# Kernel tuning notes

Measured on AMD Instinct MI355X. Metric: run time of the kernel, lower is better.

The kernel has to match this reference:

```python
import jax, jax.numpy as jnp
import numpy as np

B, T, D, H = 4, 2048, 1024, 16
Dh = D // H


def setup_inputs() -> dict:
    key = jax.random.key(0)
    ks = jax.random.split(key, 10)
    s = 0.02  # init scale for weights
    return {
        "x": jax.random.normal(ks[0], (B, T, D), jnp.float32),
        "gates": jax.random.uniform(ks[1], (B, H), jnp.float32),
        "Wq": jax.random.normal(ks[2], (D, D), jnp.float32) * s,
        "bq": jnp.zeros((D,), jnp.float32),
        "Wk": jax.random.normal(ks[3], (D, D), jnp.float32) * s,
        "bk": jnp.zeros((D,), jnp.float32),
        "Wv": jax.random.normal(ks[4], (D, D), jnp.float32) * s,
        "bv": jnp.zeros((D,), jnp.float32),
        "Wo": jax.random.normal(ks[5], (D, D), jnp.float32) * s,
        "bo": jnp.zeros((D,), jnp.float32),
    }


def reference(x, gates, Wq, bq, Wk, bk, Wv, bv, Wo, bo):
    # x: [B,T,D], gates: [B,H]. torch Linear is y = x @ W.T + b.
    b, t, d = x.shape
    h = gates.shape[1]
    dh = d // h
    q = (x @ Wq.T + bq).reshape(b, t, h, dh)
    k = (x @ Wk.T + bk).reshape(b, t, h, dh)
    v = (x @ Wv.T + bv).reshape(b, t, h, dh)
    scores = jnp.einsum('bthd,bshd->bhts', q, k) / jnp.sqrt(jnp.float32(dh))
    A = jax.nn.softmax(scores, axis=-1)
    A = A * gates[:, :, None, None]  # post-softmax per-head gate
    z = jnp.einsum('bhts,bshd->bthd', A, v).reshape(b, t, d)
    out = z @ Wo.T + bo
    return out, A
```

## Files before the change

### kernel.cpp

```cpp
#include <hip/hip_runtime.h>

#define BB 4
#define TT 2048
#define DD 1024
#define HH 16
#define DHH 64

using half8  = __attribute__((ext_vector_type(8))) _Float16;
using half4v = __attribute__((ext_vector_type(4))) _Float16;
using f32x4  = __attribute__((ext_vector_type(4))) float;

#define EXP2C 0.18033688011112042f

__device__ __forceinline__ float fexp2(float x) {
#if __has_builtin(__builtin_amdgcn_exp2f)
  return __builtin_amdgcn_exp2f(x);
#else
  return exp2f(x);
#endif
}

__device__ __forceinline__ void gload_lds16(const _Float16* g, _Float16* l) {
  __builtin_amdgcn_global_load_lds((const __attribute__((address_space(1))) void*)g,
                                   (__attribute__((address_space(3))) void*)l, 16, 0, 0);
}

__global__ void cvt_all(const float* __restrict__ x,
                        const float* __restrict__ wq, const float* __restrict__ wk,
                        const float* __restrict__ wv, const float* __restrict__ wo,
                        _Float16* __restrict__ xh,
                        _Float16* __restrict__ wqh, _Float16* __restrict__ wkh,
                        _Float16* __restrict__ wvh, _Float16* __restrict__ woh) {
  const float* s; _Float16* d; int n8, b0, nb;
  int b = blockIdx.x;
  if (b < 512) { s = x; d = xh; n8 = BB * TT * DD / 8; b0 = b; nb = 512; }
  else {
    int wsel = (b - 512) >> 6;
    b0 = (b - 512) & 63; nb = 64; n8 = DD * DD / 8;
    s = wsel == 0 ? wq : wsel == 1 ? wk : wsel == 2 ? wv : wo;
    d = wsel == 0 ? wqh : wsel == 1 ? wkh : wsel == 2 ? wvh : woh;
  }
  for (int i = b0 * 256 + threadIdx.x; i < n8; i += nb * 256) {
    const float4* p = (const float4*)(s + (size_t)i * 8);
    float4 a = p[0], bb = p[1];
    half8 h;
    h[0] = (_Float16)a.x; h[1] = (_Float16)a.y; h[2] = (_Float16)a.z; h[3] = (_Float16)a.w;
    h[4] = (_Float16)bb.x; h[5] = (_Float16)bb.y; h[6] = (_Float16)bb.z; h[7] = (_Float16)bb.w;
    *(half8*)(d + (size_t)i * 8) = h;
  }
}

template <int MODE>
__global__ __launch_bounds__(256, 2) void gemm_nt(const _Float16* __restrict__ A,
                                                  const _Float16* __restrict__ Bw,
                                                  const float* __restrict__ bias,
                                                  void* __restrict__ Cout) {
  constexpr int K = 1024;
  __shared__ _Float16 As[2][128 * 64];
  __shared__ _Float16 Bs[2][128 * 64];
  const int tid = threadIdx.x;
  const int l = tid & 63, w = tid >> 6;
  const int wm = w >> 1, wn = w & 1;
  const int lg = l >> 4, lr16 = l & 15;
  const int row0 = blockIdx.x * 128, col0 = blockIdx.y * 128;

  f32x4 acc[4][4];
#pragma unroll
  for (int i = 0; i < 4; ++i)
#pragma unroll
    for (int j = 0; j < 4; ++j) acc[i][j] = (f32x4)0.0f;

#define GEMM_STAGE(K0, BSEL)                                                        \
  _Pragma("unroll") for (int it = 0; it < 4; ++it) {                                \
    int chunk = tid + it * 256;                                                     \
    int r = chunk >> 3, pb = chunk & 7, lb = pb ^ (r & 7);                          \
    gload_lds16(A + (size_t)(row0 + r) * K + (K0) * 64 + lb * 8, As[BSEL] + chunk * 8);  \
    gload_lds16(Bw + (size_t)(col0 + r) * K + (K0) * 64 + lb * 8, Bs[BSEL] + chunk * 8); \
  }

  GEMM_STAGE(0, 0);
  int cur = 0;
  for (int k0 = 0; k0 < 16; ++k0) {
    __syncthreads();
    if (k0 < 15) GEMM_STAGE(k0 + 1, cur ^ 1);
#pragma unroll
    for (int kb = 0; kb < 2; ++kb) {
      half8 a[4], b[4];
#pragma unroll
      for (int f = 0; f < 4; ++f) {
        int ar = wm * 64 + f * 16 + lr16;
        a[f] = *(const half8*)(As[cur] + ar * 64 + ((kb * 4 + lg) ^ (ar & 7)) * 8);
        int br = wn * 64 + f * 16 + lr16;
        b[f] = *(const half8*)(Bs[cur] + br * 64 + ((kb * 4 + lg) ^ (br & 7)) * 8);
      }
#pragma unroll
      for (int i = 0; i < 4; ++i)
#pragma unroll
        for (int j = 0; j < 4; ++j)
          acc[i][j] = __builtin_amdgcn_mfma_f32_16x16x32_f16(a[i], b[j], acc[i][j], 0, 0, 0);
    }
    cur ^= 1;
  }

#pragma unroll
  for (int fi = 0; fi < 4; ++fi) {
#pragma unroll
    for (int fj = 0; fj < 4; ++fj) {
      int gi0 = row0 + wm * 64 + fi * 16 + lg * 4;
      int gj = col0 + wn * 64 + fj * 16 + lr16;
      float bj = bias[gj];
      if constexpr (MODE == 2) {
        float* O = (float*)Cout;
#pragma unroll
        for (int r = 0; r < 4; ++r) O[(size_t)(gi0 + r) * DD + gj] = acc[fi][fj][r] + bj;
      } else if constexpr (MODE == 1) {
        _Float16* O = (_Float16*)Cout;
        int b = gi0 >> 11, t0 = gi0 & 2047;
        int h = gj >> 6, dh = gj & 63;
        half4v tmp;
#pragma unroll
        for (int r = 0; r < 4; ++r) tmp[r] = (_Float16)(acc[fi][fj][r] + bj);
        *(half4v*)(O + (((size_t)(b * HH + h) * DHH + dh) * TT + t0)) = tmp;
      } else {
        _Float16* O = (_Float16*)Cout;
        int b = gi0 >> 11, t0 = gi0 & 2047;
        int h = gj >> 6, dh = gj & 63;
#pragma unroll
        for (int r = 0; r < 4; ++r)
          O[(((size_t)(b * HH + h) * TT + (t0 + r)) << 6) + dh] = (_Float16)(acc[fi][fj][r] + bj);
      }
    }
  }
}

__global__ __launch_bounds__(512, 2) void attn_kernel(const _Float16* __restrict__ qh,
                                                      const _Float16* __restrict__ kh,
                                                      const _Float16* __restrict__ vTh,
                                                      const float* __restrict__ gates,
                                                      float* __restrict__ Aout,
                                                      _Float16* __restrict__ zh) {
  __shared__ _Float16 Qs[128 * 64];
  __shared__ _Float16 Ks[2][64 * 64];
  __shared__ _Float16 Vs[2][64 * 64];
  __shared__ _Float16 Ps[128 * 64];
  const int tid = threadIdx.x;
  const int l = tid & 63, w = tid >> 6;
  const int lg = l >> 4, lr16 = l & 15;
  const int wr0 = w * 16;
  const int blk = ((int)blockIdx.x & 7) * 128 + ((int)blockIdx.x >> 3);
  const int rt = blk & 15, bh = blk >> 4;
  const _Float16* Qp = qh + (size_t)bh * TT * DHH + (size_t)rt * 128 * DHH;
  const _Float16* Kp = kh + (size_t)bh * TT * DHH;
  const _Float16* Vp = vTh + (size_t)bh * DHH * TT;
  float* Ap = Aout + (size_t)bh * TT * TT + (size_t)rt * 128 * TT;
  const float gate = gates[bh];

#pragma unroll
  for (int it = 0; it < 2; ++it) {
    int chunk = tid + it * 512;
    int r = chunk >> 3, pb = chunk & 7, lb = pb ^ (r & 7);
    gload_lds16(Qp + (size_t)r * DHH + lb * 8, Qs + chunk * 8);
  }

#define STAGE_K(CT, BSEL) {                                                   \
    int chunk = tid; int r = chunk >> 3, pb = chunk & 7, lb = pb ^ (r & 7);   \
    gload_lds16(Kp + (size_t)((CT) * 64 + r) * DHH + lb * 8, Ks[BSEL] + chunk * 8); }
#define STAGE_V(CT, BSEL) {                                                   \
    int chunk = tid; int r = chunk >> 3, pb = chunk & 7, lb = pb ^ (r & 7);   \
    gload_lds16(Vp + (size_t)r * TT + (CT) * 64 + lb * 8, Vs[BSEL] + chunk * 8); }

  STAGE_K(0, 0);
  float rs[4] = {0.f, 0.f, 0.f, 0.f};
  int cur = 0;
  for (int ct = 0; ct < 32; ++ct) {
    __syncthreads();
    if (ct < 31) STAGE_K(ct + 1, cur ^ 1);
    f32x4 s[4];
#pragma unroll
    for (int j = 0; j < 4; ++j) s[j] = (f32x4)0.0f;
#pragma unroll
    for (int kb = 0; kb < 2; ++kb) {
      int qr = wr0 + lr16;
      half8 aQ = *(const half8*)(Qs + qr * 64 + (((kb * 4 + lg) ^ (qr & 7)) * 8));
      half8 bK[4];
#pragma unroll
      for (int fc = 0; fc < 4; ++fc) {
        int kr = fc * 16 + lr16;
        bK[fc] = *(const half8*)(Ks[cur] + kr * 64 + (((kb * 4 + lg) ^ (kr & 7)) * 8));
      }
#pragma unroll
      for (int fc = 0; fc < 4; ++fc)
        s[fc] = __builtin_amdgcn_mfma_f32_16x16x32_f16(aQ, bK[fc], s[fc], 0, 0, 0);
    }
#pragma unroll
    for (int fc = 0; fc < 4; ++fc)
#pragma unroll
      for (int r = 0; r < 4; ++r) rs[r] += fexp2(s[fc][r] * EXP2C);
    cur ^= 1;
  }

  float inv[4];
#pragma unroll
  for (int r = 0; r < 4; ++r) {
    float v = rs[r];
    v += __shfl_xor(v, 1, 64);
    v += __shfl_xor(v, 2, 64);
    v += __shfl_xor(v, 4, 64);
    v += __shfl_xor(v, 8, 64);
    inv[r] = gate / v;
  }

  f32x4 z[4];
#pragma unroll
  for (int j = 0; j < 4; ++j) z[j] = (f32x4)0.0f;
  STAGE_K(0, 0);
  STAGE_V(0, 0);
  cur = 0;
  for (int ct = 0; ct < 32; ++ct) {
    __syncthreads();
    if (ct < 31) {
      STAGE_K(ct + 1, cur ^ 1);
      STAGE_V(ct + 1, cur ^ 1);
    }
    f32x4 s[4];
#pragma unroll
    for (int j = 0; j < 4; ++j) s[j] = (f32x4)0.0f;
#pragma unroll
    for (int kb = 0; kb < 2; ++kb) {
      int qr = wr0 + lr16;
      half8 aQ = *(const half8*)(Qs + qr * 64 + (((kb * 4 + lg) ^ (qr & 7)) * 8));
      half8 bK[4];
#pragma unroll
      for (int fc = 0; fc < 4; ++fc) {
        int kr = fc * 16 + lr16;
        bK[fc] = *(const half8*)(Ks[cur] + kr * 64 + (((kb * 4 + lg) ^ (kr & 7)) * 8));
      }
#pragma unroll
      for (int fc = 0; fc < 4; ++fc)
        s[fc] = __builtin_amdgcn_mfma_f32_16x16x32_f16(aQ, bK[fc], s[fc], 0, 0, 0);
    }
    const int rbase = wr0 + lg * 4;
#pragma unroll
    for (int fc = 0; fc < 4; ++fc) {
      int lc = fc * 16 + lr16;
#pragma unroll
      for (int r = 0; r < 4; ++r) {
        float av = fexp2(s[fc][r] * EXP2C) * inv[r];
        int lr = rbase + r;
        Ap[(size_t)lr * TT + (ct * 64 + lc)] = av;
        Ps[lr * 64 + (((fc * 2 + (lr16 >> 3)) ^ (lr & 7)) * 8) + (l & 7)] = (_Float16)av;
      }
    }
#pragma unroll
    for (int kb = 0; kb < 2; ++kb) {
      int pr = wr0 + lr16;
      half8 aP = *(const half8*)(Ps + pr * 64 + (((kb * 4 + lg) ^ (pr & 7)) * 8));
      half8 bV[4];
#pragma unroll
      for (int fc = 0; fc < 4; ++fc) {
        int vr = fc * 16 + lr16;
        bV[fc] = *(const half8*)(Vs[cur] + vr * 64 + (((kb * 4 + lg) ^ (vr & 7)) * 8));
      }
#pragma unroll
      for (int fc = 0; fc < 4; ++fc)
        z[fc] = __builtin_amdgcn_mfma_f32_16x16x32_f16(aP, bV[fc], z[fc], 0, 0, 0);
    }
    cur ^= 1;
  }

  const int b = bh >> 4, h = bh & 15;
  _Float16* zp = zh + ((size_t)b * TT + (size_t)rt * 128) * DD + h * 64;
  const int rbase = wr0 + lg * 4;
#pragma unroll
  for (int fc = 0; fc < 4; ++fc) {
    int d = fc * 16 + lr16;
#pragma unroll
    for (int r = 0; r < 4; ++r) zp[(size_t)(rbase + r) * DD + d] = (_Float16)z[fc][r];
  }
}

extern "C" void kernel_launch(void* const* d_in, const int* in_sizes, int n_in,
                              void* d_out, int out_size, void* d_ws, size_t ws_size,
                              hipStream_t stream) {
  const float* x     = (const float*)d_in[0];
  const float* gates = (const float*)d_in[1];
  const float* Wq    = (const float*)d_in[2];
  const float* bq    = (const float*)d_in[3];
  const float* Wk    = (const float*)d_in[4];
  const float* bk    = (const float*)d_in[5];
  const float* Wv    = (const float*)d_in[6];
  const float* bv    = (const float*)d_in[7];
  const float* Wo    = (const float*)d_in[8];
  const float* bo    = (const float*)d_in[9];

  float* out  = (float*)d_out;
  float* Aout = out + (size_t)BB * TT * DD;

  char* ws = (char*)d_ws;
  _Float16* xh  = (_Float16*)(ws);
  _Float16* Wqh = (_Float16*)(ws + (16ull << 20));
  _Float16* Wkh = (_Float16*)(ws + (18ull << 20));
  _Float16* Wvh = (_Float16*)(ws + (20ull << 20));
  _Float16* Woh = (_Float16*)(ws + (22ull << 20));
  _Float16* qh  = (_Float16*)(ws + (24ull << 20));
  _Float16* kh  = (_Float16*)(ws + (40ull << 20));
  _Float16* vTh = (_Float16*)(ws + (56ull << 20));
  _Float16* zh  = xh;

  cvt_all<<<768, 256, 0, stream>>>(x, Wq, Wk, Wv, Wo, xh, Wqh, Wkh, Wvh, Woh);

  dim3 gg(BB * TT / 128, DD / 128);
  gemm_nt<0><<<gg, 256, 0, stream>>>(xh, Wqh, bq, qh);
  gemm_nt<0><<<gg, 256, 0, stream>>>(xh, Wkh, bk, kh);
  gemm_nt<1><<<gg, 256, 0, stream>>>(xh, Wvh, bv, vTh);

  attn_kernel<<<BB * HH * (TT / 128), 512, 0, stream>>>(qh, kh, vTh, gates, Aout, zh);

  gemm_nt<2><<<gg, 256, 0, stream>>>(zh, Woh, bo, out);
}
```

Before: 477.6 us.

## Fuse QKV projections into one launch, add nontemporal stores and attention prio/sync tweaks

The three Q/K/V projection GEMMs are merged into a single launch with a 24-wide grid y dimension that selects the weight, bias and output layout per block. This cuts launch overhead and gives one larger wave of blocks. The attention PV loop moves its barrier to the end of the iteration with a partial vmcnt wait, and MFMA sections are wrapped in s_setprio. The large fp32 A output and the final output use nontemporal stores to reduce cache pollution. The hand-written waitcnt/barrier sequence is delicate: vmcnt(8) has to match the number of outstanding loads, and the stores now also count toward vmcnt.

```diff
diff --git a/kernel.cpp b/kernel.cpp
--- a/kernel.cpp
+++ b/kernel.cpp
@@ -50,11 +50,94 @@
   }
 }
 
-template <int MODE>
-__global__ __launch_bounds__(256, 2) void gemm_nt(const _Float16* __restrict__ A,
-                                                  const _Float16* __restrict__ Bw,
-                                                  const float* __restrict__ bias,
-                                                  void* __restrict__ Cout) {
+#define GEMM_STAGE(K0, BSEL)                                                        \
+  _Pragma("unroll") for (int it = 0; it < 4; ++it) {                                \
+    int chunk = tid + it * 256;                                                     \
+    int r = chunk >> 3, pb = chunk & 7, lb = pb ^ (r & 7);                          \
+    gload_lds16(A + (size_t)(row0 + r) * K + (K0) * 64 + lb * 8, As[BSEL] + chunk * 8);  \
+    gload_lds16(Bw + (size_t)(col0 + r) * K + (K0) * 64 + lb * 8, Bs[BSEL] + chunk * 8); \
+  }
+
+__global__ __launch_bounds__(256, 2) void gemm_qkv(const _Float16* __restrict__ A,
+                                                   const _Float16* __restrict__ Wqh,
+                                                   const _Float16* __restrict__ Wkh,
+                                                   const _Float16* __restrict__ Wvh,
+                                                   const float* __restrict__ bq,
+                                                   const float* __restrict__ bk,
+                                                   const float* __restrict__ bv,
+                                                   _Float16* __restrict__ qh,
+                                                   _Float16* __restrict__ kh,
+                                                   _Float16* __restrict__ vTh) {
+  constexpr int K = 1024;
+  __shared__ _Float16 As[2][128 * 64];
+  __shared__ _Float16 Bs[2][128 * 64];
+  const int tid = threadIdx.x;
+  const int l = tid & 63, w = tid >> 6;
+  const int wm = w >> 1, wn = w & 1;
+  const int lg = l >> 4, lr16 = l & 15;
+  const int wsel = (int)blockIdx.y >> 3;
+  const _Float16* Bw = wsel == 0 ? Wqh : wsel == 1 ? Wkh : Wvh;
+  const float* bias = wsel == 0 ? bq : wsel == 1 ? bk : bv;
+  const int row0 = blockIdx.x * 128, col0 = ((int)blockIdx.y & 7) * 128;
+
+  f32x4 acc[4][4];
+#pragma unroll
+  for (int i = 0; i < 4; ++i)
+#pragma unroll
+    for (int j = 0; j < 4; ++j) acc[i][j] = (f32x4)0.0f;
+
+  GEMM_STAGE(0, 0);
+  int cur = 0;
+  for (int k0 = 0; k0 < 16; ++k0) {
+    __syncthreads();
+    if (k0 < 15) GEMM_STAGE(k0 + 1, cur ^ 1);
+#pragma unroll
+    for (int kb = 0; kb < 2; ++kb) {
+      half8 a[4], b[4];
+#pragma unroll
+      for (int f = 0; f < 4; ++f) {
+        int ar = wm * 64 + f * 16 + lr16;
+        a[f] = *(const half8*)(As[cur] + ar * 64 + ((kb * 4 + lg) ^ (ar & 7)) * 8);
+        int br = wn * 64 + f * 16 + lr16;
+        b[f] = *(const half8*)(Bs[cur] + br * 64 + ((kb * 4 + lg) ^ (br & 7)) * 8);
+      }
+#pragma unroll
+      for (int i = 0; i < 4; ++i)
+#pragma unroll
+        for (int j = 0; j < 4; ++j)
+          acc[i][j] = __builtin_amdgcn_mfma_f32_16x16x32_f16(a[i], b[j], acc[i][j], 0, 0, 0);
+    }
+    cur ^= 1;
+  }
+
+#pragma unroll
+  for (int fi = 0; fi < 4; ++fi) {
+#pragma unroll
+    for (int fj = 0; fj < 4; ++fj) {
+      int gi0 = row0 + wm * 64 + fi * 16 + lg * 4;
+      int gj = col0 + wn * 64 + fj * 16 + lr16;
+      float bj = bias[gj];
+      int b = gi0 >> 11, t0 = gi0 & 2047;
+      int h = gj >> 6, dh = gj & 63;
+      if (wsel < 2) {
+        _Float16* O = wsel ? kh : qh;
+#pragma unroll
+        for (int r = 0; r < 4; ++r)
+          O[(((size_t)(b * HH + h) * TT + (t0 + r)) << 6) + dh] = (_Float16)(acc[fi][fj][r] + bj);
+      } else {
+        half4v tmp;
+#pragma unroll
+        for (int r = 0; r < 4; ++r) tmp[r] = (_Float16)(acc[fi][fj][r] + bj);
+        *(half4v*)(vTh + (((size_t)(b * HH + h) * DHH + dh) * TT + t0)) = tmp;
+      }
+    }
+  }
+}
+
+__global__ __launch_bounds__(256, 2) void gemm_out(const _Float16* __restrict__ A,
+                                                   const _Float16* __restrict__ Bw,
+                                                   const float* __restrict__ bias,
+                                                   float* __restrict__ Cout) {
   constexpr int K = 1024;
   __shared__ _Float16 As[2][128 * 64];
   __shared__ _Float16 Bs[2][128 * 64];
@@ -70,14 +153,6 @@
 #pragma unroll
     for (int j = 0; j < 4; ++j) acc[i][j] = (f32x4)0.0f;
 
-#define GEMM_STAGE(K0, BSEL)                                                        \
-  _Pragma("unroll") for (int it = 0; it < 4; ++it) {                                \
-    int chunk = tid + it * 256;                                                     \
-    int r = chunk >> 3, pb = chunk & 7, lb = pb ^ (r & 7);                          \
-    gload_lds16(A + (size_t)(row0 + r) * K + (K0) * 64 + lb * 8, As[BSEL] + chunk * 8);  \
-    gload_lds16(Bw + (size_t)(col0 + r) * K + (K0) * 64 + lb * 8, Bs[BSEL] + chunk * 8); \
-  }
-
   GEMM_STAGE(0, 0);
   int cur = 0;
   for (int k0 = 0; k0 < 16; ++k0) {
@@ -109,26 +184,9 @@
       int gi0 = row0 + wm * 64 + fi * 16 + lg * 4;
       int gj = col0 + wn * 64 + fj * 16 + lr16;
       float bj = bias[gj];
-      if constexpr (MODE == 2) {
-        float* O = (float*)Cout;
-#pragma unroll
-        for (int r = 0; r < 4; ++r) O[(size_t)(gi0 + r) * DD + gj] = acc[fi][fj][r] + bj;
-      } else if constexpr (MODE == 1) {
-        _Float16* O = (_Float16*)Cout;
-        int b = gi0 >> 11, t0 = gi0 & 2047;
-        int h = gj >> 6, dh = gj & 63;
-        half4v tmp;
-#pragma unroll
-        for (int r = 0; r < 4; ++r) tmp[r] = (_Float16)(acc[fi][fj][r] + bj);
-        *(half4v*)(O + (((size_t)(b * HH + h) * DHH + dh) * TT + t0)) = tmp;
-      } else {
-        _Float16* O = (_Float16*)Cout;
-        int b = gi0 >> 11, t0 = gi0 & 2047;
-        int h = gj >> 6, dh = gj & 63;
-#pragma unroll
-        for (int r = 0; r < 4; ++r)
-          O[(((size_t)(b * HH + h) * TT + (t0 + r)) << 6) + dh] = (_Float16)(acc[fi][fj][r] + bj);
-      }
+#pragma unroll
+      for (int r = 0; r < 4; ++r)
+        __builtin_nontemporal_store(acc[fi][fj][r] + bj, &Cout[(size_t)(gi0 + r) * DD + gj]);
     }
   }
 }
@@ -178,6 +236,7 @@
     f32x4 s[4];
 #pragma unroll
     for (int j = 0; j < 4; ++j) s[j] = (f32x4)0.0f;
+    __builtin_amdgcn_s_setprio(1);
 #pragma unroll
     for (int kb = 0; kb < 2; ++kb) {
       int qr = wr0 + lr16;
@@ -192,6 +251,7 @@
       for (int fc = 0; fc < 4; ++fc)
         s[fc] = __builtin_amdgcn_mfma_f32_16x16x32_f16(aQ, bK[fc], s[fc], 0, 0, 0);
     }
+    __builtin_amdgcn_s_setprio(0);
 #pragma unroll
     for (int fc = 0; fc < 4; ++fc)
 #pragma unroll
@@ -215,16 +275,18 @@
   for (int j = 0; j < 4; ++j) z[j] = (f32x4)0.0f;
   STAGE_K(0, 0);
   STAGE_V(0, 0);
+  asm volatile("s_waitcnt vmcnt(0)\n\ts_barrier" ::: "memory");
   cur = 0;
   for (int ct = 0; ct < 32; ++ct) {
-    __syncthreads();
     if (ct < 31) {
       STAGE_K(ct + 1, cur ^ 1);
       STAGE_V(ct + 1, cur ^ 1);
     }
+    __builtin_amdgcn_sched_barrier(0);
     f32x4 s[4];
 #pragma unroll
     for (int j = 0; j < 4; ++j) s[j] = (f32x4)0.0f;
+    __builtin_amdgcn_s_setprio(1);
 #pragma unroll
     for (int kb = 0; kb < 2; ++kb) {
       int qr = wr0 + lr16;
@@ -239,6 +301,7 @@
       for (int fc = 0; fc < 4; ++fc)
         s[fc] = __builtin_amdgcn_mfma_f32_16x16x32_f16(aQ, bK[fc], s[fc], 0, 0, 0);
     }
+    __builtin_amdgcn_s_setprio(0);
     const int rbase = wr0 + lg * 4;
 #pragma unroll
     for (int fc = 0; fc < 4; ++fc) {
@@ -247,10 +310,11 @@
       for (int r = 0; r < 4; ++r) {
         float av = fexp2(s[fc][r] * EXP2C) * inv[r];
         int lr = rbase + r;
-        Ap[(size_t)lr * TT + (ct * 64 + lc)] = av;
+        __builtin_nontemporal_store(av, &Ap[(size_t)lr * TT + (ct * 64 + lc)]);
         Ps[lr * 64 + (((fc * 2 + (lr16 >> 3)) ^ (lr & 7)) * 8) + (l & 7)] = (_Float16)av;
       }
     }
+    __builtin_amdgcn_s_setprio(1);
 #pragma unroll
     for (int kb = 0; kb < 2; ++kb) {
       int pr = wr0 + lr16;
@@ -264,6 +328,10 @@
 #pragma unroll
       for (int fc = 0; fc < 4; ++fc)
         z[fc] = __builtin_amdgcn_mfma_f32_16x16x32_f16(aP, bV[fc], z[fc], 0, 0, 0);
+    }
+    __builtin_amdgcn_s_setprio(0);
+    if (ct < 31) {
+      asm volatile("s_waitcnt vmcnt(8) lgkmcnt(0)\n\ts_barrier" ::: "memory");
     }
     cur ^= 1;
   }
@@ -309,12 +377,10 @@
 
   cvt_all<<<768, 256, 0, stream>>>(x, Wq, Wk, Wv, Wo, xh, Wqh, Wkh, Wvh, Woh);
 
-  dim3 gg(BB * TT / 128, DD / 128);
-  gemm_nt<0><<<gg, 256, 0, stream>>>(xh, Wqh, bq, qh);
-  gemm_nt<0><<<gg, 256, 0, stream>>>(xh, Wkh, bk, kh);
-  gemm_nt<1><<<gg, 256, 0, stream>>>(xh, Wvh, bv, vTh);
+  gemm_qkv<<<dim3(BB * TT / 128, 24), 256, 0, stream>>>(xh, Wqh, Wkh, Wvh, bq, bk, bv,
+                                                        qh, kh, vTh);
 
   attn_kernel<<<BB * HH * (TT / 128), 512, 0, stream>>>(qh, kh, vTh, gates, Aout, zh);
 
-  gemm_nt<2><<<gg, 256, 0, stream>>>(zh, Woh, bo, out);
-}
+  gemm_out<<<dim3(BB * TT / 128, DD / 128), 256, 0, stream>>>(zh, Woh, bo, out);
+}
```

Result: faster. 453.3 us (median of 2 runs) (-5.1%).
